# Optimization experiments

Measured on AMD Instinct MI355X. Metric: run time of the kernel, lower is better.

## Reference

```python
import jax, jax.numpy as jnp
import numpy as np
from jax import lax

HIDDEN = 256
N_FEATURES = 128
V_DIM = 64
SEQ_LEN = 1024
BATCH = 256
N_TIMESTEPS = 1024
ALPHA_INIT = 0.001


def setup_inputs() -> dict:
    key = jax.random.key(0)
    ks = jax.random.split(key, 6)
    stdv = 1.0 / np.sqrt(HIDDEN)
    u = lambda k, shape: jax.random.uniform(k, shape, jnp.float32, -stdv, stdv)
    x = jax.random.normal(ks[0], (SEQ_LEN, BATCH, N_FEATURES), jnp.float32)
    h = jax.random.normal(ks[1], (BATCH, HIDDEN), jnp.float32)
    W = u(ks[2], (N_FEATURES, HIDDEN))
    b = u(ks[3], (HIDDEN,))
    V = u(ks[4], (V_DIM, HIDDEN))
    V2 = u(ks[5], (HIDDEN, V_DIM))
    alpha = ALPHA_INIT * jnp.ones((1, N_TIMESTEPS), jnp.float32)  # K=1
    return {"x": x, "h": h, "W": W, "b": b, "V": V, "V2": V2, "alpha": alpha, "K": 1}


def reference(x, h, W, b, V, V2, alpha, K):
    # P = U = V2 @ V + I  (infite2 in the original code)
    P = jnp.matmul(V2, V) + jnp.eye(HIDDEN, dtype=W.dtype)
    # precompute input projection for all steps: [S,B,H]
    wx = jnp.einsum('sbf,fh->sbh', x, W) + b
    at = alpha[:, 0]  # self.t is never incremented in forward, so always column 0

    def step(h_prev, wx_t):
        alpha_vec = wx_t + jnp.matmul(h_prev, P)  # new_wx + b + h@U
        oldh = h_prev
        h_cur = h_prev
        for k in range(K):
            a = at[k]
            pre = jnp.matmul(jnp.matmul(h_cur, P) + alpha_vec, P)
            h_cur = a * (jnp.tanh(pre) - oldh) + (1.0 - a) * h_cur
        return h_cur, None

    h_final, _ = lax.scan(step, h, wx)
    return h_final
```

## Files before the change

kernel.cpp:

```cpp
#include <hip/hip_runtime.h>


#define HID   256
#define NF    128
#define SEQ   1024
#define SSTR  264

typedef __bf16 bf16_t;
typedef __bf16 bf16x8 __attribute__((ext_vector_type(8)));
typedef float  f32x4  __attribute__((ext_vector_type(4)));

__device__ __forceinline__ float fast_tanh(float x) {
    float e = __builtin_amdgcn_exp2f(x * 2.8853900817779268f);
    return 1.0f - 2.0f * __builtin_amdgcn_rcpf(e + 1.0f);
}

__device__ __forceinline__ int s_swz(int row) {
    return (((row >> 2) ^ (row >> 3)) & 1) << 5;
}

__global__ void k_P(const float* __restrict__ V2, const float* __restrict__ V,
                    float* __restrict__ P) {
    __shared__ float v2row[64];
    int i = blockIdx.x, j = threadIdx.x;
    if (j < 64) v2row[j] = V2[i * 64 + j];
    __syncthreads();
    float s = (i == j) ? 1.0f : 0.0f;
    #pragma unroll 4
    for (int v = 0; v < 64; ++v) s += v2row[v] * V[v * HID + j];
    P[i * HID + j] = s;
}

__global__ void k_E(const float* __restrict__ P, bf16_t* __restrict__ Et) {
    __shared__ float prow[HID];
    int i = blockIdx.x, j = threadIdx.x;
    prow[j] = P[i * HID + j];
    __syncthreads();
    float s = (i == j) ? -1.0f : 0.0f;
    #pragma unroll 4
    for (int k = 0; k < HID; ++k) s += prow[k] * P[k * HID + j];
    Et[(size_t)j * HID + i] = (bf16_t)s;
}

__global__ void k_WP(const float* __restrict__ W, const float* __restrict__ b,
                     const float* __restrict__ P,
                     bf16_t* __restrict__ WPt, float* __restrict__ bP) {
    __shared__ float row[HID];
    int i = blockIdx.x, j = threadIdx.x;
    if (i < NF) {
        row[j] = W[i * HID + j];
        __syncthreads();
        float s = 0.f;
        #pragma unroll 4
        for (int k = 0; k < HID; ++k) s += row[k] * P[k * HID + j];
        WPt[(size_t)j * NF + i] = (bf16_t)s;
    } else {
        row[j] = b[j];
        __syncthreads();
        float s = 0.f;
        #pragma unroll 4
        for (int k = 0; k < HID; ++k) s += row[k] * P[k * HID + j];
        bP[j] = s;
    }
}

__global__ __launch_bounds__(256) void k_wxp(const float* __restrict__ x,
                                             const bf16_t* __restrict__ WPt,
                                             const float* __restrict__ bP,
                                             bf16_t* __restrict__ wxp) {
    int tid = threadIdx.x;
    int lane = tid & 63, w = tid >> 6;
    int quad = lane >> 4, m = lane & 15;
    bf16x8 Bf[4][4];
    float bPv[4];
    #pragma unroll
    for (int c = 0; c < 4; ++c) {
        int col = w * 64 + c * 16 + m;
        bPv[c] = bP[col];
        const bf16_t* wp = WPt + (size_t)col * NF + quad * 8;
        #pragma unroll
        for (int kt = 0; kt < 4; ++kt)
            Bf[c][kt] = *(const bf16x8*)(wp + kt * 32);
    }
    for (int i = 0; i < 8; ++i) {
        int tile = blockIdx.x * 8 + i;
        int t = tile >> 4, g = tile & 15;
        const float* xp = x + (((size_t)t * 256 + g * 16 + m) * NF + quad * 8);
        f32x4 acc[4];
        #pragma unroll
        for (int c = 0; c < 4; ++c) acc[c] = (f32x4){bPv[c], bPv[c], bPv[c], bPv[c]};
        #pragma unroll
        for (int kt = 0; kt < 4; ++kt) {
            f32x4 xa = *(const f32x4*)(xp + kt * 32);
            f32x4 xb = *(const f32x4*)(xp + kt * 32 + 4);
            bf16x8 aa;
            #pragma unroll
            for (int j = 0; j < 4; ++j) { aa[j] = (bf16_t)xa[j]; aa[4 + j] = (bf16_t)xb[j]; }
            #pragma unroll
            for (int c = 0; c < 4; ++c)
                acc[c] = __builtin_amdgcn_mfma_f32_16x16x32_bf16(aa, Bf[c][kt], acc[c], 0, 0, 0);
        }
        bf16x8 lo, hi;
        #pragma unroll
        for (int c = 0; c < 2; ++c)
            #pragma unroll
            for (int r = 0; r < 4; ++r) {
                lo[c * 4 + r] = (bf16_t)acc[c][r];
                hi[c * 4 + r] = (bf16_t)acc[2 + c][r];
            }
        size_t tb = (size_t)tile * 4096;
        *(bf16x8*)(wxp + tb + tid * 8)        = lo;
        *(bf16x8*)(wxp + tb + 2048 + tid * 8) = hi;
    }
}

__global__ __launch_bounds__(256, 1) void k_scan_pre(const float* __restrict__ h_in,
                                                     const float* __restrict__ alpha,
                                                     const int* __restrict__ Kp,
                                                     const bf16_t* __restrict__ Et,
                                                     const bf16_t* __restrict__ wxp,
                                                     float* __restrict__ out) {
    __shared__ bf16_t S[2][16 * SSTR];
    int g = blockIdx.x;
    int tid = threadIdx.x;
    int lane = tid & 63, w = tid >> 6, quad = lane >> 4, m = lane & 15;
    int colbase = w * 64 + m;

    bf16x8 Ef[32];
    #pragma unroll
    for (int c = 0; c < 4; ++c) {
        const bf16_t* ep = Et + (size_t)(colbase + c * 16) * HID + quad * 8;
        #pragma unroll
        for (int kt = 0; kt < 8; ++kt)
            Ef[c * 8 + kt] = *(const bf16x8*)(ep + kt * 32);
    }

    const int rd_base = (m * (SSTR * 2) + quad * 16) ^ s_swz(m);
    int woff[16];
    #pragma unroll
    for (int c = 0; c < 4; ++c)
        #pragma unroll
        for (int r = 0; r < 4; ++r) {
            int row = quad * 4 + r, col = colbase + c * 16;
            woff[c * 4 + r] = ((row * SSTR + col) * 2) ^ s_swz(row);
        }

    float a = alpha[0];
    int K = Kp[0];
    if (K < 1 || K > 64) K = 1;

    float hv[16];
    #pragma unroll
    for (int c = 0; c < 4; ++c)
        #pragma unroll
        for (int r = 0; r < 4; ++r) {
            int e = c * 4 + r;
            int row = quad * 4 + r, col = colbase + c * 16;
            float v = h_in[(g * 16 + row) * HID + col];
            hv[e] = v;
            *(bf16_t*)((char*)&S[0][0] + woff[e]) = (bf16_t)(2.0f * v);
        }
    __syncthreads();

    const bf16_t* wlo = wxp + (size_t)g * 4096 + (size_t)tid * 8;
    const bf16_t* whi = wlo + 2048;
    const long WSTR = 65536;

    bf16x8 wl = *(const bf16x8*)wlo;
    bf16x8 wh = *(const bf16x8*)whi;

    if (K == 1) {
        const float A2 = 2.0f * a, B2 = 1.0f - 2.0f * a;
        float q[16];
        #pragma unroll
        for (int e = 0; e < 16; ++e) q[e] = 2.0f * hv[e];

        auto step = [&](int p, int t) {
            int tn = (t + 1 < SEQ) ? t + 1 : t;
            bf16x8 wln = *(const bf16x8*)(wlo + (long)tn * WSTR);
            bf16x8 whn = *(const bf16x8*)(whi + (long)tn * WSTR);
            f32x4 acc[4];
            #pragma unroll
            for (int r = 0; r < 4; ++r) {
                acc[0][r] = (float)wl[r];
                acc[1][r] = (float)wl[4 + r];
                acc[2][r] = (float)wh[r];
                acc[3][r] = (float)wh[4 + r];
            }
            const char* sb = (const char*)&S[p][0];
            #pragma unroll
            for (int kt = 0; kt < 8; ++kt) {
                bf16x8 af = *(const bf16x8*)(sb + rd_base + kt * 64);
                #pragma unroll
                for (int c = 0; c < 4; ++c)
                    acc[c] = __builtin_amdgcn_mfma_f32_16x16x32_bf16(af, Ef[c * 8 + kt], acc[c], 0, 0, 0);
            }
            char* swp = (char*)&S[p ^ 1][0];
            #pragma unroll
            for (int c = 0; c < 4; ++c)
                #pragma unroll
                for (int r = 0; r < 4; ++r) {
                    int e = c * 4 + r;
                    float pre = acc[c][r] + q[e];
                    float T = fast_tanh(pre);
                    float qn = fmaf(A2, T, B2 * q[e]);
                    q[e] = qn;
                    *(bf16_t*)(swp + woff[e]) = (bf16_t)qn;
                }
            __syncthreads();
            wl = wln; wh = whn;
        };
        for (int t = 0; t < SEQ; t += 2) { step(0, t); step(1, t + 1); }

        #pragma unroll
        for (int c = 0; c < 4; ++c)
            #pragma unroll
            for (int r = 0; r < 4; ++r) {
                int row = quad * 4 + r, col = colbase + c * 16;
                out[(g * 16 + row) * HID + col] = 0.5f * q[c * 4 + r];
            }
    } else {
        float hp[16], hc[16], sreg[16];
        #pragma unroll
        for (int e = 0; e < 16; ++e) { hp[e] = hv[e]; hc[e] = hv[e]; sreg[e] = 2.0f * hv[e]; }
        float one_ma = 1.0f - a;
        int p = 0;
        for (int t = 0; t < SEQ; ++t) {
            int tn = (t + 1 < SEQ) ? t + 1 : t;
            bf16x8 wln = *(const bf16x8*)(wlo + (long)tn * WSTR);
            bf16x8 whn = *(const bf16x8*)(whi + (long)tn * WSTR);
            for (int k = 0; k < K; ++k) {
                f32x4 acc[4];
                #pragma unroll
                for (int r = 0; r < 4; ++r) {
                    acc[0][r] = (float)wl[r];
                    acc[1][r] = (float)wl[4 + r];
                    acc[2][r] = (float)wh[r];
                    acc[3][r] = (float)wh[4 + r];
                }
                const char* sb = (const char*)&S[p][0];
                #pragma unroll
                for (int kt = 0; kt < 8; ++kt) {
                    bf16x8 af = *(const bf16x8*)(sb + rd_base + kt * 64);
                    #pragma unroll
                    for (int c = 0; c < 4; ++c)
                        acc[c] = __builtin_amdgcn_mfma_f32_16x16x32_bf16(af, Ef[c * 8 + kt], acc[c], 0, 0, 0);
                }
                bool last = (k == K - 1);
                char* swp = (char*)&S[p ^ 1][0];
                #pragma unroll
                for (int c = 0; c < 4; ++c)
                    #pragma unroll
                    for (int r = 0; r < 4; ++r) {
                        int e = c * 4 + r;
                        float pre = acc[c][r] + sreg[e];
                        float T = fast_tanh(pre);
                        float hn = a * (T - hp[e]) + one_ma * hc[e];
                        float sn;
                        if (last) { hp[e] = hn; hc[e] = hn; sn = 2.0f * hn; }
                        else      { hc[e] = hn; sn = hn + hp[e]; }
                        sreg[e] = sn;
                        *(bf16_t*)(swp + woff[e]) = (bf16_t)sn;
                    }
                p ^= 1;
                __syncthreads();
            }
            wl = wln; wh = whn;
        }
        #pragma unroll
        for (int c = 0; c < 4; ++c)
            #pragma unroll
            for (int r = 0; r < 4; ++r) {
                int row = quad * 4 + r, col = colbase + c * 16;
                out[(g * 16 + row) * HID + col] = hp[c * 4 + r];
            }
    }
}

__global__ __launch_bounds__(256, 1) void k_scan_fused(const float* __restrict__ h_in,
                                                 const float* __restrict__ alpha,
                                                 const int* __restrict__ Kp,
                                                 const bf16_t* __restrict__ Et,
                                                 const bf16_t* __restrict__ WPt,
                                                 const float* __restrict__ bP,
                                                 const float* __restrict__ x,
                                                 float* __restrict__ out) {
    __shared__ bf16_t S[2][16 * SSTR];
    int g = blockIdx.x;
    int tid = threadIdx.x;
    int lane = tid & 63, w = tid >> 6, quad = lane >> 4, m = lane & 15;
    int colbase = w * 64 + m;
    bf16x8 Ef[32];
    bf16x8 Wf[16];
    float bPv[4];
    #pragma unroll
    for (int c = 0; c < 4; ++c) {
        int col = colbase + c * 16;
        bPv[c] = bP[col];
        const bf16_t* ep = Et + (size_t)col * HID + quad * 8;
        #pragma unroll
        for (int kt = 0; kt < 8; ++kt)
            Ef[c * 8 + kt] = *(const bf16x8*)(ep + kt * 32);
        const bf16_t* wpp = WPt + (size_t)col * NF + quad * 8;
        #pragma unroll
        for (int kt = 0; kt < 4; ++kt)
            Wf[c * 4 + kt] = *(const bf16x8*)(wpp + kt * 32);
    }
    float hp[16], hc[16], sreg[16];
    #pragma unroll
    for (int c = 0; c < 4; ++c)
        #pragma unroll
        for (int r = 0; r < 4; ++r) {
            int e = c * 4 + r;
            int row = quad * 4 + r, col = colbase + c * 16;
            float v = h_in[(g * 16 + row) * HID + col];
            hp[e] = v; hc[e] = v; sreg[e] = 2.0f * v;
            S[0][row * SSTR + col] = (bf16_t)(2.0f * v);
        }
    float a = alpha[0];
    float one_ma = 1.0f - a;
    int K = Kp[0];
    if (K < 1 || K > 64) K = 1;
    __syncthreads();
    const float* xrow = x + ((g * 16 + m) * NF + quad * 8);
    bf16x8 xf[4];
    #pragma unroll
    for (int kt = 0; kt < 4; ++kt) {
        f32x4 xa = *(const f32x4*)(xrow + kt * 32);
        f32x4 xb = *(const f32x4*)(xrow + kt * 32 + 4);
        bf16x8 f;
        #pragma unroll
        for (int j = 0; j < 4; ++j) { f[j] = (bf16_t)xa[j]; f[4 + j] = (bf16_t)xb[j]; }
        xf[kt] = f;
    }
    int p = 0;
    for (int t = 0; t < SEQ; ++t) {
        int tn = (t + 1 < SEQ) ? t + 1 : t;
        const float* xn = xrow + (size_t)tn * (256 * NF);
        bf16x8 xnf[4];
        #pragma unroll
        for (int kt = 0; kt < 4; ++kt) {
            f32x4 xa = *(const f32x4*)(xn + kt * 32);
            f32x4 xb = *(const f32x4*)(xn + kt * 32 + 4);
            bf16x8 f;
            #pragma unroll
            for (int j = 0; j < 4; ++j) { f[j] = (bf16_t)xa[j]; f[4 + j] = (bf16_t)xb[j]; }
            xnf[kt] = f;
        }
        f32x4 wxacc[4];
        #pragma unroll
        for (int c = 0; c < 4; ++c) wxacc[c] = (f32x4){bPv[c], bPv[c], bPv[c], bPv[c]};
        #pragma unroll
        for (int kt = 0; kt < 4; ++kt)
            #pragma unroll
            for (int c = 0; c < 4; ++c)
                wxacc[c] = __builtin_amdgcn_mfma_f32_16x16x32_bf16(xf[kt], Wf[c * 4 + kt], wxacc[c], 0, 0, 0);
        for (int k = 0; k < K; ++k) {
            f32x4 acc[4];
            #pragma unroll
            for (int c = 0; c < 4; ++c) acc[c] = wxacc[c];
            const bf16_t* sbase = &S[p][m * SSTR];
            #pragma unroll
            for (int kt = 0; kt < 8; ++kt) {
                bf16x8 af = *(const bf16x8*)(sbase + kt * 32 + quad * 8);
                #pragma unroll
                for (int c = 0; c < 4; ++c)
                    acc[c] = __builtin_amdgcn_mfma_f32_16x16x32_bf16(af, Ef[c * 8 + kt], acc[c], 0, 0, 0);
            }
            bool last = (k == K - 1);
            #pragma unroll
            for (int c = 0; c < 4; ++c) {
                int col = colbase + c * 16;
                #pragma unroll
                for (int r = 0; r < 4; ++r) {
                    int e = c * 4 + r;
                    int row = quad * 4 + r;
                    float pre = acc[c][r] + sreg[e];
                    float T = fast_tanh(pre);
                    float hn = a * (T - hp[e]) + one_ma * hc[e];
                    float sn;
                    if (last) { hp[e] = hn; hc[e] = hn; sn = 2.0f * hn; }
                    else      { hc[e] = hn; sn = hn + hp[e]; }
                    sreg[e] = sn;
                    S[p ^ 1][row * SSTR + col] = (bf16_t)sn;
                }
            }
            p ^= 1;
            __syncthreads();
        }
        #pragma unroll
        for (int kt = 0; kt < 4; ++kt) xf[kt] = xnf[kt];
    }
    #pragma unroll
    for (int c = 0; c < 4; ++c)
        #pragma unroll
        for (int r = 0; r < 4; ++r) {
            int row = quad * 4 + r, col = colbase + c * 16;
            out[(g * 16 + row) * HID + col] = hp[c * 4 + r];
        }
}

extern "C" void kernel_launch(void* const* d_in, const int* in_sizes, int n_in,
                              void* d_out, int out_size, void* d_ws, size_t ws_size,
                              hipStream_t stream) {
    const float* x     = (const float*)d_in[0];
    const float* h     = (const float*)d_in[1];
    const float* W     = (const float*)d_in[2];
    const float* b     = (const float*)d_in[3];
    const float* V     = (const float*)d_in[4];
    const float* V2    = (const float*)d_in[5];
    const float* alpha = (const float*)d_in[6];
    const int*   Kp    = (const int*)d_in[7];

    char* ws = (char*)d_ws;
    float*  P   = (float*)ws;
    bf16_t* Et  = (bf16_t*)(ws + (256u << 10));
    bf16_t* WPt = (bf16_t*)(ws + (384u << 10));
    float*  bP  = (float*)(ws + (448u << 10));
    bf16_t* wxp = (bf16_t*)(ws + (512u << 10));
    size_t need = (512u << 10) + (size_t)SEQ * 16 * 512 * 8 * sizeof(bf16_t);

    hipLaunchKernelGGL(k_P,  dim3(256), dim3(256), 0, stream, V2, V, P);
    hipLaunchKernelGGL(k_E,  dim3(256), dim3(256), 0, stream, P, Et);
    hipLaunchKernelGGL(k_WP, dim3(129), dim3(256), 0, stream, W, b, P, WPt, bP);
    if (ws_size >= need) {
        hipLaunchKernelGGL(k_wxp, dim3(2048), dim3(256), 0, stream, x, WPt, bP, wxp);
        hipLaunchKernelGGL(k_scan_pre, dim3(16), dim3(256), 0, stream, h, alpha, Kp, Et, wxp, (float*)d_out);
    } else {
        hipLaunchKernelGGL(k_scan_fused, dim3(16), dim3(256), 0, stream, h, alpha, Kp, Et, WPt, bP, x, (float*)d_out);
    }
}
```

Baseline: 1.154 ms.

## Deepen wx prefetch, split MFMA accumulators, and use a lighter barrier in recurrence

In the K==1 recurrence, the input-projection loads are now prefetched two timesteps ahead instead of one, so global latency hides behind more compute. The shared-memory A fragments are loaded up front, and the MFMA chain is split into two independent accumulator sets that are summed before the tanh, which shortens the serial dependency chain. __syncthreads is replaced with an explicit lgkmcnt wait, an s_barrier and a sched_barrier to cut barrier overhead. This raises register pressure and adds a separate accumulator add, and it relies on the manual barrier being enough to order the LDS writes.

```diff
diff --git a/kernel.cpp b/kernel.cpp
--- a/kernel.cpp
+++ b/kernel.cpp
@@ -166,49 +166,65 @@
     const bf16_t* whi = wlo + 2048;
     const long WSTR = 65536;
 
-    bf16x8 wl = *(const bf16x8*)wlo;
-    bf16x8 wh = *(const bf16x8*)whi;
-
     if (K == 1) {
         const float A2 = 2.0f * a, B2 = 1.0f - 2.0f * a;
         float q[16];
         #pragma unroll
         for (int e = 0; e < 16; ++e) q[e] = 2.0f * hv[e];
 
+        bf16x8 wlA = *(const bf16x8*)(wlo);
+        bf16x8 whA = *(const bf16x8*)(whi);
+        bf16x8 wlB = *(const bf16x8*)(wlo + WSTR);
+        bf16x8 whB = *(const bf16x8*)(whi + WSTR);
+
         auto step = [&](int p, int t) {
-            int tn = (t + 1 < SEQ) ? t + 1 : t;
-            bf16x8 wln = *(const bf16x8*)(wlo + (long)tn * WSTR);
-            bf16x8 whn = *(const bf16x8*)(whi + (long)tn * WSTR);
-            f32x4 acc[4];
+            int tpf = (t + 2 < SEQ) ? t + 2 : SEQ - 1;
+            bf16x8 wlC = *(const bf16x8*)(wlo + (long)tpf * WSTR);
+            bf16x8 whC = *(const bf16x8*)(whi + (long)tpf * WSTR);
+
+            f32x4 acc[4], accb[4];
             #pragma unroll
             for (int r = 0; r < 4; ++r) {
-                acc[0][r] = (float)wl[r];
-                acc[1][r] = (float)wl[4 + r];
-                acc[2][r] = (float)wh[r];
-                acc[3][r] = (float)wh[4 + r];
-            }
+                acc[0][r] = (float)wlA[r];
+                acc[1][r] = (float)wlA[4 + r];
+                acc[2][r] = (float)whA[r];
+                acc[3][r] = (float)whA[4 + r];
+            }
+            #pragma unroll
+            for (int c = 0; c < 4; ++c) accb[c] = (f32x4){0.f, 0.f, 0.f, 0.f};
+
             const char* sb = (const char*)&S[p][0];
-            #pragma unroll
-            for (int kt = 0; kt < 8; ++kt) {
-                bf16x8 af = *(const bf16x8*)(sb + rd_base + kt * 64);
+            bf16x8 af[8];
+            #pragma unroll
+            for (int kt = 0; kt < 8; ++kt)
+                af[kt] = *(const bf16x8*)(sb + rd_base + kt * 64);
+            #pragma unroll
+            for (int kt = 0; kt < 4; ++kt)
                 #pragma unroll
                 for (int c = 0; c < 4; ++c)
-                    acc[c] = __builtin_amdgcn_mfma_f32_16x16x32_bf16(af, Ef[c * 8 + kt], acc[c], 0, 0, 0);
-            }
+                    acc[c] = __builtin_amdgcn_mfma_f32_16x16x32_bf16(af[kt], Ef[c * 8 + kt], acc[c], 0, 0, 0);
+            #pragma unroll
+            for (int kt = 4; kt < 8; ++kt)
+                #pragma unroll
+                for (int c = 0; c < 4; ++c)
+                    accb[c] = __builtin_amdgcn_mfma_f32_16x16x32_bf16(af[kt], Ef[c * 8 + kt], accb[c], 0, 0, 0);
+
             char* swp = (char*)&S[p ^ 1][0];
             #pragma unroll
             for (int c = 0; c < 4; ++c)
                 #pragma unroll
                 for (int r = 0; r < 4; ++r) {
                     int e = c * 4 + r;
-                    float pre = acc[c][r] + q[e];
+                    float pre = (acc[c][r] + accb[c][r]) + q[e];
                     float T = fast_tanh(pre);
                     float qn = fmaf(A2, T, B2 * q[e]);
                     q[e] = qn;
                     *(bf16_t*)(swp + woff[e]) = (bf16_t)qn;
                 }
-            __syncthreads();
-            wl = wln; wh = whn;
+            asm volatile("s_waitcnt lgkmcnt(0)" ::: "memory");
+            __builtin_amdgcn_s_barrier();
+            __builtin_amdgcn_sched_barrier(0);
+            wlA = wlB; whA = whB; wlB = wlC; whB = whC;
         };
         for (int t = 0; t < SEQ; t += 2) { step(0, t); step(1, t + 1); }
 
@@ -224,6 +240,8 @@
         #pragma unroll
         for (int e = 0; e < 16; ++e) { hp[e] = hv[e]; hc[e] = hv[e]; sreg[e] = 2.0f * hv[e]; }
         float one_ma = 1.0f - a;
+        bf16x8 wl = *(const bf16x8*)(wlo);
+        bf16x8 wh = *(const bf16x8*)(whi);
         int p = 0;
         for (int t = 0; t < SEQ; ++t) {
             int tn = (t + 1 < SEQ) ? t + 1 : t;
```

Measured after the change: 1.095 ms. 5.1% less time.

## Process two 16-row batch tiles per scan block to overlap serial chains

Applied to the files above, without the earlier changes.

The scan kernel now gives each workgroup two independent 16-row batch tiles (8 blocks instead of 16). Each step interleaves MFMAs and tanh updates for both tiles, so one chain's latency can hide behind the other's. The per-step __syncthreads is replaced with an explicit lgkmcnt wait plus s_barrier and a sched_barrier. This halves the number of CUs used and doubles register pressure (more accumulators and state), which risks spills or longer per-step time.

```diff
diff --git a/kernel.cpp b/kernel.cpp
--- a/kernel.cpp
+++ b/kernel.cpp
@@ -5,6 +5,7 @@
 #define NF    128
 #define SEQ   1024
 #define SSTR  264
+#define PLB   (16 * SSTR * 2)
 
 typedef __bf16 bf16_t;
 typedef __bf16 bf16x8 __attribute__((ext_vector_type(8)));
@@ -120,7 +121,7 @@
                                                      const bf16_t* __restrict__ Et,
                                                      const bf16_t* __restrict__ wxp,
                                                      float* __restrict__ out) {
-    __shared__ bf16_t S[2][16 * SSTR];
+    __shared__ bf16_t S[2 * 2 * 16 * SSTR];
     int g = blockIdx.x;
     int tid = threadIdx.x;
     int lane = tid & 63, w = tid >> 6, quad = lane >> 4, m = lane & 15;
@@ -149,131 +150,178 @@
     int K = Kp[0];
     if (K < 1 || K > 64) K = 1;
 
-    float hv[16];
-    #pragma unroll
-    for (int c = 0; c < 4; ++c)
-        #pragma unroll
-        for (int r = 0; r < 4; ++r) {
-            int e = c * 4 + r;
-            int row = quad * 4 + r, col = colbase + c * 16;
-            float v = h_in[(g * 16 + row) * HID + col];
-            hv[e] = v;
-            *(bf16_t*)((char*)&S[0][0] + woff[e]) = (bf16_t)(2.0f * v);
-        }
+    char* const sbase = (char*)&S[0];
+
+    float q[32];
+    #pragma unroll
+    for (int pi = 0; pi < 2; ++pi)
+        #pragma unroll
+        for (int c = 0; c < 4; ++c)
+            #pragma unroll
+            for (int r = 0; r < 4; ++r) {
+                int e = c * 4 + r;
+                int row = quad * 4 + r, col = colbase + c * 16;
+                float v = h_in[((g * 2 + pi) * 16 + row) * HID + col];
+                q[pi * 16 + e] = 2.0f * v;
+                *(bf16_t*)(sbase + pi * PLB + woff[e]) = (bf16_t)(2.0f * v);
+            }
     __syncthreads();
 
-    const bf16_t* wlo = wxp + (size_t)g * 4096 + (size_t)tid * 8;
-    const bf16_t* whi = wlo + 2048;
+    const bf16_t* wlo0 = wxp + (size_t)(g * 2 + 0) * 4096 + (size_t)tid * 8;
+    const bf16_t* wlo1 = wxp + (size_t)(g * 2 + 1) * 4096 + (size_t)tid * 8;
     const long WSTR = 65536;
-
-    bf16x8 wl = *(const bf16x8*)wlo;
-    bf16x8 wh = *(const bf16x8*)whi;
 
     if (K == 1) {
         const float A2 = 2.0f * a, B2 = 1.0f - 2.0f * a;
-        float q[16];
-        #pragma unroll
-        for (int e = 0; e < 16; ++e) q[e] = 2.0f * hv[e];
-
-        auto step = [&](int p, int t) {
+
+        bf16x8 c0l = *(const bf16x8*)(wlo0);
+        bf16x8 c0h = *(const bf16x8*)(wlo0 + 2048);
+        bf16x8 c1l = *(const bf16x8*)(wlo1);
+        bf16x8 c1h = *(const bf16x8*)(wlo1 + 2048);
+
+        auto step = [&](int P, int t) {
             int tn = (t + 1 < SEQ) ? t + 1 : t;
-            bf16x8 wln = *(const bf16x8*)(wlo + (long)tn * WSTR);
-            bf16x8 whn = *(const bf16x8*)(whi + (long)tn * WSTR);
-            f32x4 acc[4];
+            bf16x8 n0l = *(const bf16x8*)(wlo0 + (long)tn * WSTR);
+            bf16x8 n0h = *(const bf16x8*)(wlo0 + (long)tn * WSTR + 2048);
+            bf16x8 n1l = *(const bf16x8*)(wlo1 + (long)tn * WSTR);
+            bf16x8 n1h = *(const bf16x8*)(wlo1 + (long)tn * WSTR + 2048);
+
+            f32x4 acc0[4], acc1[4];
             #pragma unroll
             for (int r = 0; r < 4; ++r) {
-                acc[0][r] = (float)wl[r];
-                acc[1][r] = (float)wl[4 + r];
-                acc[2][r] = (float)wh[r];
-                acc[3][r] = (float)wh[4 + r];
-            }
-            const char* sb = (const char*)&S[p][0];
+                acc0[0][r] = (float)c0l[r];  acc0[1][r] = (float)c0l[4 + r];
+                acc0[2][r] = (float)c0h[r];  acc0[3][r] = (float)c0h[4 + r];
+                acc1[0][r] = (float)c1l[r];  acc1[1][r] = (float)c1l[4 + r];
+                acc1[2][r] = (float)c1h[r];  acc1[3][r] = (float)c1h[4 + r];
+            }
+            const char* sb0 = sbase + P * (2 * PLB);
+            const char* sb1 = sb0 + PLB;
             #pragma unroll
             for (int kt = 0; kt < 8; ++kt) {
-                bf16x8 af = *(const bf16x8*)(sb + rd_base + kt * 64);
+                bf16x8 a0 = *(const bf16x8*)(sb0 + rd_base + kt * 64);
+                bf16x8 a1 = *(const bf16x8*)(sb1 + rd_base + kt * 64);
                 #pragma unroll
                 for (int c = 0; c < 4; ++c)
-                    acc[c] = __builtin_amdgcn_mfma_f32_16x16x32_bf16(af, Ef[c * 8 + kt], acc[c], 0, 0, 0);
-            }
-            char* swp = (char*)&S[p ^ 1][0];
+                    acc0[c] = __builtin_amdgcn_mfma_f32_16x16x32_bf16(a0, Ef[c * 8 + kt], acc0[c], 0, 0, 0);
+                #pragma unroll
+                for (int c = 0; c < 4; ++c)
+                    acc1[c] = __builtin_amdgcn_mfma_f32_16x16x32_bf16(a1, Ef[c * 8 + kt], acc1[c], 0, 0, 0);
+            }
+            char* sw0 = sbase + (P ^ 1) * (2 * PLB);
+            char* sw1 = sw0 + PLB;
             #pragma unroll
             for (int c = 0; c < 4; ++c)
                 #pragma unroll
                 for (int r = 0; r < 4; ++r) {
                     int e = c * 4 + r;
-                    float pre = acc[c][r] + q[e];
+                    float pre = acc0[c][r] + q[e];
                     float T = fast_tanh(pre);
                     float qn = fmaf(A2, T, B2 * q[e]);
                     q[e] = qn;
-                    *(bf16_t*)(swp + woff[e]) = (bf16_t)qn;
-                }
-            __syncthreads();
-            wl = wln; wh = whn;
+                    *(bf16_t*)(sw0 + woff[e]) = (bf16_t)qn;
+                }
+            #pragma unroll
+            for (int c = 0; c < 4; ++c)
+                #pragma unroll
+                for (int r = 0; r < 4; ++r) {
+                    int e = c * 4 + r;
+                    float pre = acc1[c][r] + q[16 + e];
+                    float T = fast_tanh(pre);
+                    float qn = fmaf(A2, T, B2 * q[16 + e]);
+                    q[16 + e] = qn;
+                    *(bf16_t*)(sw1 + woff[e]) = (bf16_t)qn;
+                }
+            asm volatile("s_waitcnt lgkmcnt(0)" ::: "memory");
+            __builtin_amdgcn_s_barrier();
+            __builtin_amdgcn_sched_barrier(0);
+            c0l = n0l; c0h = n0h; c1l = n1l; c1h = n1h;
         };
         for (int t = 0; t < SEQ; t += 2) { step(0, t); step(1, t + 1); }
 
         #pragma unroll
-        for (int c = 0; c < 4; ++c)
-            #pragma unroll
-            for (int r = 0; r < 4; ++r) {
-                int row = quad * 4 + r, col = colbase + c * 16;
-                out[(g * 16 + row) * HID + col] = 0.5f * q[c * 4 + r];
-            }
+        for (int pi = 0; pi < 2; ++pi)
+            #pragma unroll
+            for (int c = 0; c < 4; ++c)
+                #pragma unroll
+                for (int r = 0; r < 4; ++r) {
+                    int row = quad * 4 + r, col = colbase + c * 16;
+                    out[((g * 2 + pi) * 16 + row) * HID + col] = 0.5f * q[pi * 16 + c * 4 + r];
+                }
     } else {
-        float hp[16], hc[16], sreg[16];
-        #pragma unroll
-        for (int e = 0; e < 16; ++e) { hp[e] = hv[e]; hc[e] = hv[e]; sreg[e] = 2.0f * hv[e]; }
+        float hp[32], hc[32], sreg[32];
+        #pragma unroll
+        for (int e = 0; e < 32; ++e) { hp[e] = 0.5f * q[e]; hc[e] = hp[e]; sreg[e] = q[e]; }
         float one_ma = 1.0f - a;
+        bf16x8 c0l = *(const bf16x8*)(wlo0);
+        bf16x8 c0h = *(const bf16x8*)(wlo0 + 2048);
+        bf16x8 c1l = *(const bf16x8*)(wlo1);
+        bf16x8 c1h = *(const bf16x8*)(wlo1 + 2048);
         int p = 0;
         for (int t = 0; t < SEQ; ++t) {
             int tn = (t + 1 < SEQ) ? t + 1 : t;
-            bf16x8 wln = *(const bf16x8*)(wlo + (long)tn * WSTR);
-            bf16x8 whn = *(const bf16x8*)(whi + (long)tn * WSTR);
+            bf16x8 n0l = *(const bf16x8*)(wlo0 + (long)tn * WSTR);
+            bf16x8 n0h = *(const bf16x8*)(wlo0 + (long)tn * WSTR + 2048);
+            bf16x8 n1l = *(const bf16x8*)(wlo1 + (long)tn * WSTR);
+            bf16x8 n1h = *(const bf16x8*)(wlo1 + (long)tn * WSTR + 2048);
             for (int k = 0; k < K; ++k) {
-                f32x4 acc[4];
-                #pragma unroll
-                for (int r = 0; r < 4; ++r) {
-                    acc[0][r] = (float)wl[r];
-                    acc[1][r] = (float)wl[4 + r];
-                    acc[2][r] = (float)wh[r];
-                    acc[3][r] = (float)wh[4 + r];
-                }
-                const char* sb = (const char*)&S[p][0];
+                f32x4 acc0[4], acc1[4];
+                #pragma unroll
+                for (int r = 0; r < 4; ++r) {
+                    acc0[0][r] = (float)c0l[r];  acc0[1][r] = (float)c0l[4 + r];
+                    acc0[2][r] = (float)c0h[r];  acc0[3][r] = (float)c0h[4 + r];
+                    acc1[0][r] = (float)c1l[r];  acc1[1][r] = (float)c1l[4 + r];
+                    acc1[2][r] = (float)c1h[r];  acc1[3][r] = (float)c1h[4 + r];
+                }
+                const char* sb0 = sbase + p * (2 * PLB);
+                const char* sb1 = sb0 + PLB;
                 #pragma unroll
                 for (int kt = 0; kt < 8; ++kt) {
-                    bf16x8 af = *(const bf16x8*)(sb + rd_base + kt * 64);
+                    bf16x8 a0 = *(const bf16x8*)(sb0 + rd_base + kt * 64);
+                    bf16x8 a1 = *(const bf16x8*)(sb1 + rd_base + kt * 64);
                     #pragma unroll
                     for (int c = 0; c < 4; ++c)
-                        acc[c] = __builtin_amdgcn_mfma_f32_16x16x32_bf16(af, Ef[c * 8 + kt], acc[c], 0, 0, 0);
+                        acc0[c] = __builtin_amdgcn_mfma_f32_16x16x32_bf16(a0, Ef[c * 8 + kt], acc0[c], 0, 0, 0);
+                    #pragma unroll
+                    for (int c = 0; c < 4; ++c)
+                        acc1[c] = __builtin_amdgcn_mfma_f32_16x16x32_bf16(a1, Ef[c * 8 + kt], acc1[c], 0, 0, 0);
                 }
                 bool last = (k == K - 1);
-                char* swp = (char*)&S[p ^ 1][0];
-                #pragma unroll
-                for (int c = 0; c < 4; ++c)
+                char* sw0 = sbase + (p ^ 1) * (2 * PLB);
+                char* sw1 = sw0 + PLB;
+                #pragma unroll
+                for (int pi = 0; pi < 2; ++pi) {
+                    char* sw = pi ? sw1 : sw0;
                     #pragma unroll
-                    for (int r = 0; r < 4; ++r) {
-                        int e = c * 4 + r;
-                        float pre = acc[c][r] + sreg[e];
-                        float T = fast_tanh(pre);
-                        float hn = a * (T - hp[e]) + one_ma * hc[e];
-                        float sn;
-                        if (last) { hp[e] = hn; hc[e] = hn; sn = 2.0f * hn; }
-                        else      { hc[e] = hn; sn = hn + hp[e]; }
-                        sreg[e] = sn;
-                        *(bf16_t*)(swp + woff[e]) = (bf16_t)sn;
-                    }
+                    for (int c = 0; c < 4; ++c)
+                        #pragma unroll
+                        for (int r = 0; r < 4; ++r) {
+                            int e = c * 4 + r;
+                            int ee = pi * 16 + e;
+                            f32x4* acc = pi ? acc1 : acc0;
+                            float pre = acc[c][r] + sreg[ee];
+                            float T = fast_tanh(pre);
+                            float hn = a * (T - hp[ee]) + one_ma * hc[ee];
+                            float sn;
+                            if (last) { hp[ee] = hn; hc[ee] = hn; sn = 2.0f * hn; }
+                            else      { hc[ee] = hn; sn = hn + hp[ee]; }
+                            sreg[ee] = sn;
+                            *(bf16_t*)(sw + woff[e]) = (bf16_t)sn;
+                        }
+                }
                 p ^= 1;
                 __syncthreads();
             }
-            wl = wln; wh = whn;
-        }
-        #pragma unroll
-        for (int c = 0; c < 4; ++c)
-            #pragma unroll
-            for (int r = 0; r < 4; ++r) {
-                int row = quad * 4 + r, col = colbase + c * 16;
-                out[(g * 16 + row) * HID + col] = hp[c * 4 + r];
-            }
+            c0l = n0l; c0h = n0h; c1l = n1l; c1h = n1h;
+        }
+        #pragma unroll
+        for (int pi = 0; pi < 2; ++pi)
+            #pragma unroll
+            for (int c = 0; c < 4; ++c)
+                #pragma unroll
+                for (int r = 0; r < 4; ++r) {
+                    int row = quad * 4 + r, col = colbase + c * 16;
+                    out[((g * 2 + pi) * 16 + row) * HID + col] = hp[pi * 16 + c * 4 + r];
+                }
     }
 }
 
@@ -425,7 +473,7 @@
     hipLaunchKernelGGL(k_WP, dim3(129), dim3(256), 0, stream, W, b, P, WPt, bP);
     if (ws_size >= need) {
         hipLaunchKernelGGL(k_wxp, dim3(2048), dim3(256), 0, stream, x, WPt, bP, wxp);
-        hipLaunchKernelGGL(k_scan_pre, dim3(16), dim3(256), 0, stream, h, alpha, Kp, Et, wxp, (float*)d_out);
+        hipLaunchKernelGGL(k_scan_pre, dim3(8), dim3(256), 0, stream, h, alpha, Kp, Et, wxp, (float*)d_out);
     } else {
         hipLaunchKernelGGL(k_scan_fused, dim3(16), dim3(256), 0, stream, h, alpha, Kp, Et, WPt, bP, x, (float*)d_out);
     }
```

Result: slower. 1.963 ms (+70.2%).
